# Kernel optimization log

Measured on AMD Instinct MI355X. Metric: run time of the kernel, lower is better.

The kernel has to match this reference:

```python
import jax, jax.numpy as jnp
import numpy as np

H = 128   # hidden_size
E = 100   # embedding/input_size
V = 1000  # vocabulary_size
FD = 512  # feature_extractor_dim
N, TQ, TA = 512, 64, 64


def _cell(x, h, c, Wih, Whh, b):
    # PyTorch LSTM cell, gate order i,f,g,o; b = b_ih + b_hh fused.
    z = x @ Wih.T + h @ Whh.T + b
    i, f, g, o = jnp.split(z, 4, axis=-1)
    c = jax.nn.sigmoid(f) * c + jax.nn.sigmoid(i) * jnp.tanh(g)
    h = jax.nn.sigmoid(o) * jnp.tanh(c)
    return h, c


def setup_inputs() -> dict:
    key = jax.random.key(0)
    ks = iter(jax.random.split(key, 40))
    def w(shape, s=0.08):
        return (s * jax.random.normal(next(ks), shape)).astype(jnp.float32)
    inp = {
        "questions": jax.random.randint(next(ks), (N, TQ), 0, V),
        "answers": jax.random.randint(next(ks), (N, TA), 0, V),
        "answer_lens": jax.random.randint(next(ks), (N,), 1, TA + 1),
        "img": w((FD,), 1.0),  # pre-extracted image features (feature_extractor = identity)
        "emb": w((V, E), 0.1),
    }
    for p in ("enc", "dec"):
        inp[p + "_Wih0"] = w((4 * H, E)); inp[p + "_Whh0"] = w((4 * H, H)); inp[p + "_b0"] = w((4 * H,))
        inp[p + "_Wih1"] = w((4 * H, H)); inp[p + "_Whh1"] = w((4 * H, H)); inp[p + "_b1"] = w((4 * H,))
    inp["Wk"] = w((H, H)); inp["bk"] = w((H,))
    inp["Wout"] = w((V, 3 * H + FD)); inp["bout"] = w((V,))
    return inp


def reference(questions, answers, answer_lens, img, emb,
              enc_Wih0, enc_Whh0, enc_b0, enc_Wih1, enc_Whh1, enc_b1,
              dec_Wih0, dec_Whh0, dec_b0, dec_Wih1, dec_Whh1, dec_b1,
              Wk, bk, Wout, bout):
    n, tq = questions.shape
    # ---- encode: 2-layer LSTM over all questions (batched), keys projection ----
    qe = emb[questions]                               # [N,TQ,E]
    z = jnp.zeros((n, H), emb.dtype)
    def enc_step(carry, x_t):
        h0, c0, h1, c1 = carry
        h0, c0 = _cell(x_t, h0, c0, enc_Wih0, enc_Whh0, enc_b0)
        h1, c1 = _cell(h0, h1, c1, enc_Wih1, enc_Whh1, enc_b1)
        return (h0, c0, h1, c1), h1
    (eh0, ec0, eh1, ec1), outs = jax.lax.scan(enc_step, (z, z, z, z), qe.swapaxes(0, 1))
    keys = outs.swapaxes(0, 1) @ Wk.T + bk            # [N,TQ,H]; decode uses keys as values too

    # ---- decode: sequential over questions (history carry), scan over timesteps ----
    ae = emb[answers]                                  # [N,TA,E]
    mask = (jnp.arange(answers.shape[1])[None, :] < answer_lens[:, None]).astype(emb.dtype)

    def q_step(history, xs):
        emb_q, k_q, h0, c0, h1, c1, m_q = xs
        def t_step(carry, x_t):
            h0, c0, h1, c1 = carry
            h0, c0 = _cell(x_t, h0, c0, dec_Wih0, dec_Whh0, dec_b0)
            h1, c1 = _cell(h0, h1, c1, dec_Wih1, dec_Whh1, dec_b1)
            ctx = jax.nn.softmax(k_q @ h1) @ k_q       # dot-product attention, v := k (as in source)
            feat = jnp.concatenate([h1, ctx, history, img], axis=-1)  # [3H+FD]
            return (h0, c0, h1, c1), feat @ Wout.T + bout
        carry, logits = jax.lax.scan(t_step, (h0, c0, h1, c1), emb_q)
        return carry[2], logits * m_q[:, None]         # history <- last-layer h; mask ragged tail

    _, logits = jax.lax.scan(q_step, jnp.zeros((H,), emb.dtype),
                             (ae, keys, eh0, ec0, eh1, ec1, mask))
    return logits                                      # [N,TA,V], zero-padded past answer_lens
```

## Files before the change

kernel.cpp:

```cpp
#include <hip/hip_runtime.h>
#include <stdint.h>

#define HD   128
#define ED   100
#define VD   1000
#define FDV  512
#define NS   512
#define TT   64
#define MT   (NS*TT)

typedef __attribute__((ext_vector_type(8))) short  short8;
typedef __attribute__((ext_vector_type(4))) float  f32x4;

typedef const __attribute__((address_space(1))) uint16_t* gas_u16;
typedef __attribute__((address_space(3))) uint16_t*       las_u16;

__device__ __forceinline__ float blo(uint32_t u){ return __uint_as_float(u << 16); }
__device__ __forceinline__ float bhi(uint32_t u){ return __uint_as_float(u & 0xffff0000u); }
__device__ __forceinline__ uint16_t f2bf(float f){
  uint32_t x = __float_as_uint(f);
  return (uint16_t)((x + 0x7fffu + ((x >> 16) & 1u)) >> 16);
}
__device__ __forceinline__ float sigf(float x){ return 1.f/(1.f+__expf(-x)); }
__device__ __forceinline__ float ftanh(float x){
  float ax = fabsf(x);
  float e = __expf(-2.f*ax);
  float t = (1.f - e) / (1.f + e);
  return copysignf(t, x);
}
__device__ __forceinline__ void lds_barrier(){
  asm volatile("s_waitcnt lgkmcnt(0)" ::: "memory");
  __builtin_amdgcn_s_barrier();
}

struct ConvJob { const float* s; uint16_t* d; int R, R0, C, Cp; };
struct ConvJobs { ConvJob j[12]; };

__global__ void k_convert(ConvJobs jobs){
  int stride = gridDim.x * blockDim.x;
  int tid0 = blockIdx.x * blockDim.x + threadIdx.x;
  for (int ji = 0; ji < 12; ++ji){
    const ConvJob jb = jobs.j[ji];
    int total = jb.R * jb.Cp;
    for (int i = tid0; i < total; i += stride){
      int r = i / jb.Cp, c = i - r*jb.Cp;
      float v = (r < jb.R0 && c < jb.C) ? jb.s[(size_t)r*jb.C + c] : 0.f;
      jb.d[i] = f2bf(v);
    }
  }
}

template<int MODE>
__global__ __launch_bounds__(256) void k_gemm(
    const uint16_t* __restrict__ A, const uint16_t* __restrict__ W,
    const float* __restrict__ bias, void* __restrict__ out,
    int N, int K, const int* __restrict__ lens, const int* __restrict__ tok)
{
  __shared__ __align__(16) uint16_t lsA[128][32];
  __shared__ __align__(16) uint16_t lsB[128][32];
  const int tid = threadIdx.x;
  const int n0 = blockIdx.x * 128, m0 = blockIdx.y * 128;
  const int l = tid & 63, w = tid >> 6;
  const int wm = (w >> 1) * 64, wn = (w & 1) * 64;
  const int fr = l & 15, fo = (l >> 4) * 8;
  const int srow = w*16 + (l >> 2);
  const int sce  = (l & 3) * 8;
  const int ar0 = m0 + srow, ar1 = m0 + 64 + srow;
  const size_t ab0 = (tok ? (size_t)tok[ar0] : (size_t)ar0) * K;
  const size_t ab1 = (tok ? (size_t)tok[ar1] : (size_t)ar1) * K;
  f32x4 acc[4][4] = {};
  for (int kt = 0; kt < K; kt += 32) {
    {
      __builtin_amdgcn_global_load_lds(
          (gas_u16)(A + ab0 + kt + sce),
          (las_u16)(&lsA[0][0] + w*512), 16, 0, 0);
      __builtin_amdgcn_global_load_lds(
          (gas_u16)(W + (size_t)(n0 + srow) * K + kt + sce),
          (las_u16)(&lsB[0][0] + w*512), 16, 0, 0);
      __builtin_amdgcn_global_load_lds(
          (gas_u16)(A + ab1 + kt + sce),
          (las_u16)(&lsA[0][0] + w*512 + 2048), 16, 0, 0);
      __builtin_amdgcn_global_load_lds(
          (gas_u16)(W + (size_t)(n0 + 64 + srow) * K + kt + sce),
          (las_u16)(&lsB[0][0] + w*512 + 2048), 16, 0, 0);
    }
    __syncthreads();
    short8 af[4], bfv[4];
    #pragma unroll
    for (int i = 0; i < 4; ++i) af[i]  = *(const short8*)(&lsA[wm + i*16 + fr][fo]);
    #pragma unroll
    for (int j = 0; j < 4; ++j) bfv[j] = *(const short8*)(&lsB[wn + j*16 + fr][fo]);
    #pragma unroll
    for (int i = 0; i < 4; ++i)
      #pragma unroll
      for (int j = 0; j < 4; ++j)
        acc[i][j] = __builtin_amdgcn_mfma_f32_16x16x32_bf16(af[i], bfv[j], acc[i][j], 0, 0, 0);
    __syncthreads();
  }
  const int r0 = (l >> 4) * 4, cc = l & 15;
  #pragma unroll
  for (int j = 0; j < 4; ++j) {
    int col = n0 + wn + j*16 + cc;
    if (col >= N) continue;
    float bv = bias[col];
    #pragma unroll
    for (int i = 0; i < 4; ++i) {
      #pragma unroll
      for (int r = 0; r < 4; ++r) {
        int row = m0 + wm + i*16 + r0 + r;
        float v = acc[i][j][r] + bv;
        if (MODE == 3) {
          int t = row & 63, n = row >> 6;
          size_t prow = ((size_t)(n >> 4)*64 + (size_t)t)*16 + (n & 15);
          ((uint16_t*)out)[prow * 512 + col] = f2bf(v);
        } else if (MODE == 2) {
          int t = row & 63, n = row >> 6;
          if (t >= lens[n]) v = 0.f;
          ((float*)out)[(size_t)row * N + col] = v;
        } else {
          ((float*)out)[(size_t)row * N + col] = v;
        }
      }
    }
  }
}

__global__ __launch_bounds__(512) void k_lstm_mfma(
    const uint16_t* __restrict__ X,
    const uint16_t* __restrict__ Whh,
    const float* __restrict__ h0i, const float* __restrict__ c0i,
    uint16_t* __restrict__ hout,
    float* __restrict__ hfin, float* __restrict__ cfin)
{
  __shared__ __align__(16) uint16_t hbuf[2][16][136];
  const int n0 = blockIdx.x * 16;
  const int w = threadIdx.x >> 6, l = threadIdx.x & 63;
  const int s = l & 15;
  const int hi4 = l >> 4;
  const int j0 = w*16 + hi4*4;

  short8 afr[4][4];
  #pragma unroll
  for (int g = 0; g < 4; ++g)
    #pragma unroll
    for (int kk = 0; kk < 4; ++kk)
      afr[g][kk] = *(const short8*)(Whh + (size_t)(g*128 + w*16 + s)*128 + kk*32 + hi4*8);

  f32x4 cst = {0.f, 0.f, 0.f, 0.f};
  if (c0i) cst = *(const f32x4*)(c0i + (size_t)(n0+s)*128 + j0);
  {
    uint16_t hb[4] = {0,0,0,0};
    if (h0i) {
      float4 hv = *(const float4*)(h0i + (size_t)(n0+s)*128 + j0);
      hb[0]=f2bf(hv.x); hb[1]=f2bf(hv.y); hb[2]=f2bf(hv.z); hb[3]=f2bf(hv.w);
    }
    *(uint2*)(&hbuf[0][s][j0]) = *(const uint2*)hb;
  }
  __syncthreads();

  const uint16_t* Xp = X + (size_t)blockIdx.x * TT * 8192 + s*512 + j0;
  uint2 xv[4], xvn[4];
  #pragma unroll
  for (int g = 0; g < 4; ++g) xv[g] = *(const uint2*)(Xp + g*128);

  float hfv[4] = {0.f,0.f,0.f,0.f};
  for (int t = 0; t < TT; ++t) {
    const int rb = t & 1;
    if (t + 1 < TT) {
      const uint16_t* Xn = Xp + (size_t)(t+1)*8192;
      #pragma unroll
      for (int g = 0; g < 4; ++g) xvn[g] = *(const uint2*)(Xn + g*128);
    }
    short8 bfr[4];
    #pragma unroll
    for (int kk = 0; kk < 4; ++kk)
      bfr[kk] = *(const short8*)(&hbuf[rb][s][kk*32 + hi4*8]);
    f32x4 acc[4] = {{0.f,0.f,0.f,0.f},{0.f,0.f,0.f,0.f},{0.f,0.f,0.f,0.f},{0.f,0.f,0.f,0.f}};
    #pragma unroll
    for (int kk = 0; kk < 4; ++kk)
      #pragma unroll
      for (int g = 0; g < 4; ++g)
        acc[g] = __builtin_amdgcn_mfma_f32_16x16x32_bf16(afr[g][kk], bfr[kk], acc[g], 0, 0, 0);
    uint16_t hb[4];
    #pragma unroll
    for (int r = 0; r < 4; ++r) {
      uint32_t wi = (r & 2) ? xv[0].y : xv[0].x;
      uint32_t wf = (r & 2) ? xv[1].y : xv[1].x;
      uint32_t wg = (r & 2) ? xv[2].y : xv[2].x;
      uint32_t wo = (r & 2) ? xv[3].y : xv[3].x;
      float zi = acc[0][r] + ((r & 1) ? bhi(wi) : blo(wi));
      float zf = acc[1][r] + ((r & 1) ? bhi(wf) : blo(wf));
      float zg = acc[2][r] + ((r & 1) ? bhi(wg) : blo(wg));
      float zo = acc[3][r] + ((r & 1) ? bhi(wo) : blo(wo));
      float cn = sigf(zf) * cst[r] + sigf(zi) * ftanh(zg);
      float h  = sigf(zo) * ftanh(cn);
      cst[r] = cn;
      hfv[r] = h;
      hb[r] = f2bf(h);
    }
    *(uint2*)(&hbuf[rb ^ 1][s][j0]) = *(const uint2*)hb;
    *(uint2*)(hout + ((size_t)(n0+s)*TT + t)*HD + j0) = *(const uint2*)hb;
    if (t + 1 < TT) {
      #pragma unroll
      for (int g = 0; g < 4; ++g) xv[g] = xvn[g];
    }
    lds_barrier();
  }
  if (hfin) *(float4*)(hfin + (size_t)(n0+s)*128 + j0) = make_float4(hfv[0],hfv[1],hfv[2],hfv[3]);
  if (cfin) *(float4*)(cfin + (size_t)(n0+s)*128 + j0) = make_float4(cst[0],cst[1],cst[2],cst[3]);
}

__global__ __launch_bounds__(256) void k_attn(
    const float* __restrict__ keys,
    const uint16_t* __restrict__ h1,
    const uint16_t* __restrict__ imgb,
    uint16_t* __restrict__ feat)
{
  __shared__ float ks[64][129];
  __shared__ float ps[4][64];
  const int n = blockIdx.x;
  for (int i = threadIdx.x; i < 64*128; i += 256)
    ks[i >> 7][i & 127] = keys[(size_t)n*8192 + i];
  const int w = threadIdx.x >> 6, l = threadIdx.x & 63;
  uint32_t hd = 0;
  if (n > 0) hd = ((const uint32_t*)(h1 + ((size_t)(n-1)*64 + 63)*128))[l];
  const uint4 iv = ((const uint4*)imgb)[l];
  __syncthreads();
  for (int tt = 0; tt < 16; ++tt) {
    const int t = tt*4 + w;
    const size_t m = (size_t)n*64 + t;
    const uint4* hp = (const uint4*)(h1 + m*128);
    float s = 0.f;
    #pragma unroll
    for (int k = 0; k < 16; ++k) {
      uint4 hv = hp[k];
      s += ks[l][8*k+0]*blo(hv.x) + ks[l][8*k+1]*bhi(hv.x)
         + ks[l][8*k+2]*blo(hv.y) + ks[l][8*k+3]*bhi(hv.y)
         + ks[l][8*k+4]*blo(hv.z) + ks[l][8*k+5]*bhi(hv.z)
         + ks[l][8*k+6]*blo(hv.w) + ks[l][8*k+7]*bhi(hv.w);
    }
    float mx = s;
    #pragma unroll
    for (int o = 32; o; o >>= 1) mx = fmaxf(mx, __shfl_xor(mx, o));
    float p = __expf(s - mx);
    float sm = p;
    #pragma unroll
    for (int o = 32; o; o >>= 1) sm += __shfl_xor(sm, o);
    p /= sm;
    ps[w][l] = p;
    float c0 = 0.f, c1 = 0.f;
    #pragma unroll
    for (int q = 0; q < 64; ++q) {
      float pq = ps[w][q];
      c0 += pq * ks[q][l];
      c1 += pq * ks[q][l + 64];
    }
    uint16_t* fr_ = feat + m*896;
    ((uint32_t*)fr_)[l] = ((const uint32_t*)(h1 + m*128))[l];
    fr_[128 + l] = f2bf(c0);
    fr_[192 + l] = f2bf(c1);
    ((uint32_t*)(fr_ + 256))[l] = hd;
    ((uint4*)(fr_ + 384))[l] = iv;
  }
}

extern "C" void kernel_launch(void* const* d_in, const int* in_sizes, int n_in,
                              void* d_out, int out_size, void* d_ws, size_t ws_size,
                              hipStream_t stream) {
  const int*   questions = (const int*)d_in[0];
  const int*   answers   = (const int*)d_in[1];
  const int*   lens      = (const int*)d_in[2];
  const float* img       = (const float*)d_in[3];
  const float* emb       = (const float*)d_in[4];
  const float* eWih0 = (const float*)d_in[5],  *eWhh0 = (const float*)d_in[6],  *eB0 = (const float*)d_in[7];
  const float* eWih1 = (const float*)d_in[8],  *eWhh1 = (const float*)d_in[9],  *eB1 = (const float*)d_in[10];
  const float* dWih0 = (const float*)d_in[11], *dWhh0 = (const float*)d_in[12], *dB0 = (const float*)d_in[13];
  const float* dWih1 = (const float*)d_in[14], *dWhh1 = (const float*)d_in[15], *dB1 = (const float*)d_in[16];
  const float* Wk   = (const float*)d_in[17], *bk   = (const float*)d_in[18];
  const float* Wout = (const float*)d_in[19], *bout = (const float*)d_in[20];

  char* ws = (char*)d_ws;
  size_t off = 0;
  auto alloc = [&](size_t n)->char* {
    char* p = ws + off; off += (n + 255) & ~(size_t)255; return p;
  };
  uint16_t* embP  = (uint16_t*)alloc((size_t)VD*128*2);
  uint16_t* wih0e = (uint16_t*)alloc(512*128*2);
  uint16_t* whh0e = (uint16_t*)alloc(512*128*2);
  uint16_t* wih1e = (uint16_t*)alloc(512*128*2);
  uint16_t* whh1e = (uint16_t*)alloc(512*128*2);
  uint16_t* wih0d = (uint16_t*)alloc(512*128*2);
  uint16_t* whh0d = (uint16_t*)alloc(512*128*2);
  uint16_t* wih1d = (uint16_t*)alloc(512*128*2);
  uint16_t* whh1d = (uint16_t*)alloc(512*128*2);
  uint16_t* wkb   = (uint16_t*)alloc(128*128*2);
  uint16_t* woutb = (uint16_t*)alloc((size_t)1024*896*2);
  uint16_t* imgb  = (uint16_t*)alloc(512*2);
  uint16_t* Xbuf  = (uint16_t*)alloc((size_t)MT*512*2);
  uint16_t* hA    = (uint16_t*)alloc((size_t)MT*128*2);
  uint16_t* h1b   = (uint16_t*)alloc((size_t)MT*128*2);
  float*    keysf = (float*)   alloc((size_t)MT*128*4);
  uint16_t* feat  = (uint16_t*)alloc((size_t)MT*896*2);
  float* eh0 = (float*)alloc(NS*128*4);
  float* ec0 = (float*)alloc(NS*128*4);
  float* eh1 = (float*)alloc(NS*128*4);
  float* ec1 = (float*)alloc(NS*128*4);
  if (off > ws_size) return;

  ConvJobs jobs;
  jobs.j[0]  = {emb,   embP,  VD,  VD,  ED,  128};
  jobs.j[1]  = {eWih0, wih0e, 512, 512, ED,  128};
  jobs.j[2]  = {eWhh0, whh0e, 512, 512, 128, 128};
  jobs.j[3]  = {eWih1, wih1e, 512, 512, 128, 128};
  jobs.j[4]  = {eWhh1, whh1e, 512, 512, 128, 128};
  jobs.j[5]  = {dWih0, wih0d, 512, 512, ED,  128};
  jobs.j[6]  = {dWhh0, whh0d, 512, 512, 128, 128};
  jobs.j[7]  = {dWih1, wih1d, 512, 512, 128, 128};
  jobs.j[8]  = {dWhh1, whh1d, 512, 512, 128, 128};
  jobs.j[9]  = {Wk,    wkb,   128, 128, 128, 128};
  jobs.j[10] = {Wout,  woutb, 1024, VD, 896, 896};
  jobs.j[11] = {img,   imgb,  1,   1,   512, 512};
  hipLaunchKernelGGL(k_convert, dim3(1024), dim3(256), 0, stream, jobs);

  hipLaunchKernelGGL(k_gemm<3>, dim3(4, MT/128), dim3(256), 0, stream, embP, wih0e, eB0, Xbuf, 512, 128, nullptr, questions);
  hipLaunchKernelGGL(k_lstm_mfma, dim3(NS/16), dim3(512), 0, stream, Xbuf, whh0e, (const float*)nullptr, (const float*)nullptr, hA, eh0, ec0);
  hipLaunchKernelGGL(k_gemm<3>, dim3(4, MT/128), dim3(256), 0, stream, hA, wih1e, eB1, Xbuf, 512, 128, nullptr, nullptr);
  hipLaunchKernelGGL(k_lstm_mfma, dim3(NS/16), dim3(512), 0, stream, Xbuf, whh1e, (const float*)nullptr, (const float*)nullptr, h1b, eh1, ec1);
  hipLaunchKernelGGL(k_gemm<0>, dim3(1, MT/128), dim3(256), 0, stream, h1b, wkb, bk, keysf, 128, 128, nullptr, nullptr);

  hipLaunchKernelGGL(k_gemm<3>, dim3(4, MT/128), dim3(256), 0, stream, embP, wih0d, dB0, Xbuf, 512, 128, nullptr, answers);
  hipLaunchKernelGGL(k_lstm_mfma, dim3(NS/16), dim3(512), 0, stream, Xbuf, whh0d, eh0, ec0, hA, (float*)nullptr, (float*)nullptr);
  hipLaunchKernelGGL(k_gemm<3>, dim3(4, MT/128), dim3(256), 0, stream, hA, wih1d, dB1, Xbuf, 512, 128, nullptr, nullptr);
  hipLaunchKernelGGL(k_lstm_mfma, dim3(NS/16), dim3(512), 0, stream, Xbuf, whh1d, eh1, ec1, h1b, (float*)nullptr, (float*)nullptr);

  hipLaunchKernelGGL(k_attn, dim3(NS), dim3(256), 0, stream, keysf, h1b, imgb, feat);
  hipLaunchKernelGGL(k_gemm<2>, dim3(8, MT/128), dim3(256), 0, stream, feat, woutb, bout, d_out, VD, 896, lens, nullptr);
}
```

Measured before the change: 890.7 us.

## Fuse both LSTM layers into one wavefront-pipelined recurrent kernel

Replaces the separate layer-0 LSTM, layer-1 input GEMM and layer-1 LSTM launches with a single kernel that runs both layers, skewed by one timestep. Each step computes layer 1 at t-1 from the layer-0 h already in LDS, so the layer-1 input projection is done in-kernel with register-resident Wih1 fragments. This removes the intermediate hA round-trip through global memory, one GEMM launch and one LSTM launch per encoder and decoder. In exchange it triples the weight fragments held in registers (occupancy/spill risk) and roughly doubles the MFMA work on each serial step. Final h states are now rounded through bf16.

```diff
diff --git a/kernel.cpp b/kernel.cpp
--- a/kernel.cpp
+++ b/kernel.cpp
@@ -125,89 +125,152 @@
   }
 }
 
-__global__ __launch_bounds__(512) void k_lstm_mfma(
+__global__ __launch_bounds__(512) void k_lstm2(
     const uint16_t* __restrict__ X,
-    const uint16_t* __restrict__ Whh,
+    const uint16_t* __restrict__ Whh0,
+    const uint16_t* __restrict__ Wih1,
+    const uint16_t* __restrict__ Whh1,
+    const float* __restrict__ B1,
     const float* __restrict__ h0i, const float* __restrict__ c0i,
+    const float* __restrict__ h1i, const float* __restrict__ c1i,
     uint16_t* __restrict__ hout,
-    float* __restrict__ hfin, float* __restrict__ cfin)
+    float* __restrict__ h0f, float* __restrict__ c0f,
+    float* __restrict__ h1f, float* __restrict__ c1f)
 {
-  __shared__ __align__(16) uint16_t hbuf[2][16][136];
+  __shared__ __align__(16) uint16_t hb0[2][16][136];
+  __shared__ __align__(16) uint16_t hb1[2][16][136];
   const int n0 = blockIdx.x * 16;
   const int w = threadIdx.x >> 6, l = threadIdx.x & 63;
   const int s = l & 15;
   const int hi4 = l >> 4;
   const int j0 = w*16 + hi4*4;
 
-  short8 afr[4][4];
+  short8 w0fr[4][4], wi1fr[4][4], wh1fr[4][4];
   #pragma unroll
   for (int g = 0; g < 4; ++g)
     #pragma unroll
-    for (int kk = 0; kk < 4; ++kk)
-      afr[g][kk] = *(const short8*)(Whh + (size_t)(g*128 + w*16 + s)*128 + kk*32 + hi4*8);
-
-  f32x4 cst = {0.f, 0.f, 0.f, 0.f};
-  if (c0i) cst = *(const f32x4*)(c0i + (size_t)(n0+s)*128 + j0);
+    for (int kk = 0; kk < 4; ++kk) {
+      const size_t ro = (size_t)(g*128 + w*16 + s)*128 + kk*32 + hi4*8;
+      w0fr[g][kk]  = *(const short8*)(Whh0 + ro);
+      wi1fr[g][kk] = *(const short8*)(Wih1 + ro);
+      wh1fr[g][kk] = *(const short8*)(Whh1 + ro);
+    }
+  f32x4 b1v[4];
+  #pragma unroll
+  for (int g = 0; g < 4; ++g) b1v[g] = *(const f32x4*)(B1 + g*128 + j0);
+
+  f32x4 cst0 = {0.f,0.f,0.f,0.f}, cst1 = {0.f,0.f,0.f,0.f};
+  if (c0i) cst0 = *(const f32x4*)(c0i + (size_t)(n0+s)*128 + j0);
+  if (c1i) cst1 = *(const f32x4*)(c1i + (size_t)(n0+s)*128 + j0);
   {
-    uint16_t hb[4] = {0,0,0,0};
+    uint16_t a[4] = {0,0,0,0}, b[4] = {0,0,0,0};
     if (h0i) {
       float4 hv = *(const float4*)(h0i + (size_t)(n0+s)*128 + j0);
-      hb[0]=f2bf(hv.x); hb[1]=f2bf(hv.y); hb[2]=f2bf(hv.z); hb[3]=f2bf(hv.w);
-    }
-    *(uint2*)(&hbuf[0][s][j0]) = *(const uint2*)hb;
+      a[0]=f2bf(hv.x); a[1]=f2bf(hv.y); a[2]=f2bf(hv.z); a[3]=f2bf(hv.w);
+    }
+    if (h1i) {
+      float4 hv = *(const float4*)(h1i + (size_t)(n0+s)*128 + j0);
+      b[0]=f2bf(hv.x); b[1]=f2bf(hv.y); b[2]=f2bf(hv.z); b[3]=f2bf(hv.w);
+    }
+    *(uint2*)(&hb0[1][s][j0]) = *(const uint2*)a;
+    *(uint2*)(&hb1[1][s][j0]) = *(const uint2*)b;
   }
   __syncthreads();
 
   const uint16_t* Xp = X + (size_t)blockIdx.x * TT * 8192 + s*512 + j0;
-  uint2 xv[4], xvn[4];
+  uint16_t* hop = hout + (size_t)(n0+s)*TT*HD + j0;
+
+  uint2 xv[4];
   #pragma unroll
   for (int g = 0; g < 4; ++g) xv[g] = *(const uint2*)(Xp + g*128);
 
-  float hfv[4] = {0.f,0.f,0.f,0.f};
-  for (int t = 0; t < TT; ++t) {
-    const int rb = t & 1;
-    if (t + 1 < TT) {
-      const uint16_t* Xn = Xp + (size_t)(t+1)*8192;
-      #pragma unroll
-      for (int g = 0; g < 4; ++g) xvn[g] = *(const uint2*)(Xn + g*128);
-    }
-    short8 bfr[4];
+  for (int t = 0; t <= TT; ++t) {
+    const int ra = (t+1)&1, wa = t&1;
+    short8 bfr0[4];
     #pragma unroll
     for (int kk = 0; kk < 4; ++kk)
-      bfr[kk] = *(const short8*)(&hbuf[rb][s][kk*32 + hi4*8]);
-    f32x4 acc[4] = {{0.f,0.f,0.f,0.f},{0.f,0.f,0.f,0.f},{0.f,0.f,0.f,0.f},{0.f,0.f,0.f,0.f}};
-    #pragma unroll
-    for (int kk = 0; kk < 4; ++kk)
-      #pragma unroll
-      for (int g = 0; g < 4; ++g)
-        acc[g] = __builtin_amdgcn_mfma_f32_16x16x32_bf16(afr[g][kk], bfr[kk], acc[g], 0, 0, 0);
-    uint16_t hb[4];
-    #pragma unroll
-    for (int r = 0; r < 4; ++r) {
-      uint32_t wi = (r & 2) ? xv[0].y : xv[0].x;
-      uint32_t wf = (r & 2) ? xv[1].y : xv[1].x;
-      uint32_t wg = (r & 2) ? xv[2].y : xv[2].x;
-      uint32_t wo = (r & 2) ? xv[3].y : xv[3].x;
-      float zi = acc[0][r] + ((r & 1) ? bhi(wi) : blo(wi));
-      float zf = acc[1][r] + ((r & 1) ? bhi(wf) : blo(wf));
-      float zg = acc[2][r] + ((r & 1) ? bhi(wg) : blo(wg));
-      float zo = acc[3][r] + ((r & 1) ? bhi(wo) : blo(wo));
-      float cn = sigf(zf) * cst[r] + sigf(zi) * ftanh(zg);
-      float h  = sigf(zo) * ftanh(cn);
-      cst[r] = cn;
-      hfv[r] = h;
-      hb[r] = f2bf(h);
-    }
-    *(uint2*)(&hbuf[rb ^ 1][s][j0]) = *(const uint2*)hb;
-    *(uint2*)(hout + ((size_t)(n0+s)*TT + t)*HD + j0) = *(const uint2*)hb;
-    if (t + 1 < TT) {
-      #pragma unroll
-      for (int g = 0; g < 4; ++g) xv[g] = xvn[g];
+      bfr0[kk] = *(const short8*)(&hb0[ra][s][kk*32 + hi4*8]);
+
+    f32x4 acc1[4] = {{0,0,0,0},{0,0,0,0},{0,0,0,0},{0,0,0,0}};
+    if (t > 0) {
+      short8 bfr1[4];
+      #pragma unroll
+      for (int kk = 0; kk < 4; ++kk)
+        bfr1[kk] = *(const short8*)(&hb1[wa][s][kk*32 + hi4*8]);
+      #pragma unroll
+      for (int kk = 0; kk < 4; ++kk)
+        #pragma unroll
+        for (int g = 0; g < 4; ++g)
+          acc1[g] = __builtin_amdgcn_mfma_f32_16x16x32_bf16(wh1fr[g][kk], bfr1[kk], acc1[g], 0, 0, 0);
+      #pragma unroll
+      for (int kk = 0; kk < 4; ++kk)
+        #pragma unroll
+        for (int g = 0; g < 4; ++g)
+          acc1[g] = __builtin_amdgcn_mfma_f32_16x16x32_bf16(wi1fr[g][kk], bfr0[kk], acc1[g], 0, 0, 0);
+    }
+    f32x4 acc0[4] = {{0,0,0,0},{0,0,0,0},{0,0,0,0},{0,0,0,0}};
+    if (t < TT) {
+      #pragma unroll
+      for (int kk = 0; kk < 4; ++kk)
+        #pragma unroll
+        for (int g = 0; g < 4; ++g)
+          acc0[g] = __builtin_amdgcn_mfma_f32_16x16x32_bf16(w0fr[g][kk], bfr0[kk], acc0[g], 0, 0, 0);
+    }
+    if (t > 0) {
+      uint16_t hb[4];
+      #pragma unroll
+      for (int r = 0; r < 4; ++r) {
+        float zi = acc1[0][r] + b1v[0][r];
+        float zf = acc1[1][r] + b1v[1][r];
+        float zg = acc1[2][r] + b1v[2][r];
+        float zo = acc1[3][r] + b1v[3][r];
+        float cn = sigf(zf) * cst1[r] + sigf(zi) * ftanh(zg);
+        float h  = sigf(zo) * ftanh(cn);
+        cst1[r] = cn;
+        hb[r] = f2bf(h);
+      }
+      *(uint2*)(&hb1[ra][s][j0]) = *(const uint2*)hb;
+      *(uint2*)(hop + (size_t)(t-1)*HD) = *(const uint2*)hb;
+    }
+    if (t < TT) {
+      uint16_t hb[4];
+      #pragma unroll
+      for (int r = 0; r < 4; ++r) {
+        uint32_t wi = (r & 2) ? xv[0].y : xv[0].x;
+        uint32_t wf = (r & 2) ? xv[1].y : xv[1].x;
+        uint32_t wg = (r & 2) ? xv[2].y : xv[2].x;
+        uint32_t wo = (r & 2) ? xv[3].y : xv[3].x;
+        float zi = acc0[0][r] + ((r & 1) ? bhi(wi) : blo(wi));
+        float zf = acc0[1][r] + ((r & 1) ? bhi(wf) : blo(wf));
+        float zg = acc0[2][r] + ((r & 1) ? bhi(wg) : blo(wg));
+        float zo = acc0[3][r] + ((r & 1) ? bhi(wo) : blo(wo));
+        float cn = sigf(zf) * cst0[r] + sigf(zi) * ftanh(zg);
+        float h  = sigf(zo) * ftanh(cn);
+        cst0[r] = cn;
+        hb[r] = f2bf(h);
+      }
+      *(uint2*)(&hb0[wa][s][j0]) = *(const uint2*)hb;
+      if (t + 1 < TT) {
+        const uint16_t* Xn = Xp + (size_t)(t+1)*8192;
+        #pragma unroll
+        for (int g = 0; g < 4; ++g) xv[g] = *(const uint2*)(Xn + g*128);
+      }
     }
     lds_barrier();
   }
-  if (hfin) *(float4*)(hfin + (size_t)(n0+s)*128 + j0) = make_float4(hfv[0],hfv[1],hfv[2],hfv[3]);
-  if (cfin) *(float4*)(cfin + (size_t)(n0+s)*128 + j0) = make_float4(cst[0],cst[1],cst[2],cst[3]);
+
+  if (h0f) {
+    uint2 a = *(const uint2*)(&hb0[1][s][j0]);
+    uint2 b = *(const uint2*)(&hb1[1][s][j0]);
+    const uint16_t* ap = (const uint16_t*)&a;
+    const uint16_t* bp = (const uint16_t*)&b;
+    float4 h0v = make_float4(blo(ap[0]), blo(ap[1]), blo(ap[2]), blo(ap[3]));
+    float4 h1v = make_float4(blo(bp[0]), blo(bp[1]), blo(bp[2]), blo(bp[3]));
+    *(float4*)(h0f + (size_t)(n0+s)*128 + j0) = h0v;
+    *(float4*)(h1f + (size_t)(n0+s)*128 + j0) = h1v;
+    *(f32x4*)(c0f + (size_t)(n0+s)*128 + j0) = cst0;
+    *(f32x4*)(c1f + (size_t)(n0+s)*128 + j0) = cst1;
+  }
 }
 
 __global__ __launch_bounds__(256) void k_attn(
@@ -297,7 +360,6 @@
   uint16_t* woutb = (uint16_t*)alloc((size_t)1024*896*2);
   uint16_t* imgb  = (uint16_t*)alloc(512*2);
   uint16_t* Xbuf  = (uint16_t*)alloc((size_t)MT*512*2);
-  uint16_t* hA    = (uint16_t*)alloc((size_t)MT*128*2);
   uint16_t* h1b   = (uint16_t*)alloc((size_t)MT*128*2);
   float*    keysf = (float*)   alloc((size_t)MT*128*4);
   uint16_t* feat  = (uint16_t*)alloc((size_t)MT*896*2);
@@ -323,15 +385,17 @@
   hipLaunchKernelGGL(k_convert, dim3(1024), dim3(256), 0, stream, jobs);
 
   hipLaunchKernelGGL(k_gemm<3>, dim3(4, MT/128), dim3(256), 0, stream, embP, wih0e, eB0, Xbuf, 512, 128, nullptr, questions);
-  hipLaunchKernelGGL(k_lstm_mfma, dim3(NS/16), dim3(512), 0, stream, Xbuf, whh0e, (const float*)nullptr, (const float*)nullptr, hA, eh0, ec0);
-  hipLaunchKernelGGL(k_gemm<3>, dim3(4, MT/128), dim3(256), 0, stream, hA, wih1e, eB1, Xbuf, 512, 128, nullptr, nullptr);
-  hipLaunchKernelGGL(k_lstm_mfma, dim3(NS/16), dim3(512), 0, stream, Xbuf, whh1e, (const float*)nullptr, (const float*)nullptr, h1b, eh1, ec1);
+  hipLaunchKernelGGL(k_lstm2, dim3(NS/16), dim3(512), 0, stream,
+                     Xbuf, whh0e, wih1e, whh1e, eB1,
+                     (const float*)nullptr, (const float*)nullptr, (const float*)nullptr, (const float*)nullptr,
+                     h1b, eh0, ec0, eh1, ec1);
   hipLaunchKernelGGL(k_gemm<0>, dim3(1, MT/128), dim3(256), 0, stream, h1b, wkb, bk, keysf, 128, 128, nullptr, nullptr);
 
   hipLaunchKernelGGL(k_gemm<3>, dim3(4, MT/128), dim3(256), 0, stream, embP, wih0d, dB0, Xbuf, 512, 128, nullptr, answers);
-  hipLaunchKernelGGL(k_lstm_mfma, dim3(NS/16), dim3(512), 0, stream, Xbuf, whh0d, eh0, ec0, hA, (float*)nullptr, (float*)nullptr);
-  hipLaunchKernelGGL(k_gemm<3>, dim3(4, MT/128), dim3(256), 0, stream, hA, wih1d, dB1, Xbuf, 512, 128, nullptr, nullptr);
-  hipLaunchKernelGGL(k_lstm_mfma, dim3(NS/16), dim3(512), 0, stream, Xbuf, whh1d, eh1, ec1, h1b, (float*)nullptr, (float*)nullptr);
+  hipLaunchKernelGGL(k_lstm2, dim3(NS/16), dim3(512), 0, stream,
+                     Xbuf, whh0d, wih1d, whh1d, dB1,
+                     eh0, ec0, eh1, ec1,
+                     h1b, (float*)nullptr, (float*)nullptr, (float*)nullptr, (float*)nullptr);
 
   hipLaunchKernelGGL(k_attn, dim3(NS), dim3(256), 0, stream, keysf, h1b, imgb, feat);
   hipLaunchKernelGGL(k_gemm<2>, dim3(8, MT/128), dim3(256), 0, stream, feat, woutb, bout, d_out, VD, 896, lens, nullptr);
```

After: 1.033 ms. 16.0% more time.

## Process two interleaved sequence groups per LSTM block to hide recurrence latency

Applied to the files above, without the earlier changes.

The recurrent LSTM kernel now has each block handle 32 sequences as two independent 16-row groups. Their MFMA chains and gate math are interleaved so each group's dependent latency can hide the other's, and the time loop is unrolled by two with a double-buffered X prefetch. This halves the grid to 16 blocks, leaving fewer CUs busy, and raises register pressure. Whether per-step latency hiding beats the lost parallelism is uncertain.

```diff
diff --git a/kernel.cpp b/kernel.cpp
--- a/kernel.cpp
+++ b/kernel.cpp
@@ -125,18 +125,96 @@
   }
 }
 
-__global__ __launch_bounds__(512) void k_lstm_mfma(
+template<int RB>
+__device__ __forceinline__ void lstm_step(
+    const short8 (&afr)[4][4],
+    uint16_t (*hb)[2][16][136],
+    int s, int hi4, int j0, int t,
+    const uint16_t* __restrict__ XA, const uint16_t* __restrict__ XB,
+    uint2 (&xa)[4], uint2 (&xb)[4],
+    f32x4& cstA, f32x4& cstB,
+    uint16_t* __restrict__ hoA, uint16_t* __restrict__ hoB,
+    float (&hfA)[4], float (&hfB)[4])
+{
+  short8 bA[4], bB[4];
+  #pragma unroll
+  for (int kk = 0; kk < 4; ++kk) {
+    bA[kk] = *(const short8*)(&hb[RB][0][s][kk*32 + hi4*8]);
+    bB[kk] = *(const short8*)(&hb[RB][1][s][kk*32 + hi4*8]);
+  }
+  f32x4 aA[4] = {{0,0,0,0},{0,0,0,0},{0,0,0,0},{0,0,0,0}};
+  f32x4 aB[4] = {{0,0,0,0},{0,0,0,0},{0,0,0,0},{0,0,0,0}};
+  #pragma unroll
+  for (int kk = 0; kk < 4; ++kk) {
+    #pragma unroll
+    for (int g = 0; g < 4; ++g)
+      aA[g] = __builtin_amdgcn_mfma_f32_16x16x32_bf16(afr[g][kk], bA[kk], aA[g], 0, 0, 0);
+    #pragma unroll
+    for (int g = 0; g < 4; ++g)
+      aB[g] = __builtin_amdgcn_mfma_f32_16x16x32_bf16(afr[g][kk], bB[kk], aB[g], 0, 0, 0);
+  }
+  {
+    uint16_t hv[4];
+    #pragma unroll
+    for (int r = 0; r < 4; ++r) {
+      uint32_t wi = (r & 2) ? xa[0].y : xa[0].x;
+      uint32_t wf = (r & 2) ? xa[1].y : xa[1].x;
+      uint32_t wg = (r & 2) ? xa[2].y : xa[2].x;
+      uint32_t wo = (r & 2) ? xa[3].y : xa[3].x;
+      float zi = aA[0][r] + ((r & 1) ? bhi(wi) : blo(wi));
+      float zf = aA[1][r] + ((r & 1) ? bhi(wf) : blo(wf));
+      float zg = aA[2][r] + ((r & 1) ? bhi(wg) : blo(wg));
+      float zo = aA[3][r] + ((r & 1) ? bhi(wo) : blo(wo));
+      float cn = sigf(zf) * cstA[r] + sigf(zi) * ftanh(zg);
+      float h  = sigf(zo) * ftanh(cn);
+      cstA[r] = cn; hfA[r] = h; hv[r] = f2bf(h);
+    }
+    *(uint2*)(&hb[RB ^ 1][0][s][j0]) = *(const uint2*)hv;
+    *(uint2*)(hoA + (size_t)t*HD) = *(const uint2*)hv;
+    if (t + 2 < TT) {
+      const uint16_t* Xn = XA + (size_t)(t+2)*8192;
+      #pragma unroll
+      for (int g = 0; g < 4; ++g) xa[g] = *(const uint2*)(Xn + g*128);
+    }
+  }
+  {
+    uint16_t hv[4];
+    #pragma unroll
+    for (int r = 0; r < 4; ++r) {
+      uint32_t wi = (r & 2) ? xb[0].y : xb[0].x;
+      uint32_t wf = (r & 2) ? xb[1].y : xb[1].x;
+      uint32_t wg = (r & 2) ? xb[2].y : xb[2].x;
+      uint32_t wo = (r & 2) ? xb[3].y : xb[3].x;
+      float zi = aB[0][r] + ((r & 1) ? bhi(wi) : blo(wi));
+      float zf = aB[1][r] + ((r & 1) ? bhi(wf) : blo(wf));
+      float zg = aB[2][r] + ((r & 1) ? bhi(wg) : blo(wg));
+      float zo = aB[3][r] + ((r & 1) ? bhi(wo) : blo(wo));
+      float cn = sigf(zf) * cstB[r] + sigf(zi) * ftanh(zg);
+      float h  = sigf(zo) * ftanh(cn);
+      cstB[r] = cn; hfB[r] = h; hv[r] = f2bf(h);
+    }
+    *(uint2*)(&hb[RB ^ 1][1][s][j0]) = *(const uint2*)hv;
+    *(uint2*)(hoB + (size_t)t*HD) = *(const uint2*)hv;
+    if (t + 2 < TT) {
+      const uint16_t* Xn = XB + (size_t)(t+2)*8192;
+      #pragma unroll
+      for (int g = 0; g < 4; ++g) xb[g] = *(const uint2*)(Xn + g*128);
+    }
+  }
+  lds_barrier();
+}
+
+__global__ __launch_bounds__(512, 2) void k_lstm_d(
     const uint16_t* __restrict__ X,
     const uint16_t* __restrict__ Whh,
     const float* __restrict__ h0i, const float* __restrict__ c0i,
     uint16_t* __restrict__ hout,
     float* __restrict__ hfin, float* __restrict__ cfin)
 {
-  __shared__ __align__(16) uint16_t hbuf[2][16][136];
-  const int n0 = blockIdx.x * 16;
+  __shared__ __align__(16) uint16_t hbuf[2][2][16][136];
+  const int b = blockIdx.x;
   const int w = threadIdx.x >> 6, l = threadIdx.x & 63;
-  const int s = l & 15;
-  const int hi4 = l >> 4;
+  const int s = l & 15, hi4 = l >> 4;
   const int j0 = w*16 + hi4*4;
 
   short8 afr[4][4];
@@ -146,68 +224,49 @@
     for (int kk = 0; kk < 4; ++kk)
       afr[g][kk] = *(const short8*)(Whh + (size_t)(g*128 + w*16 + s)*128 + kk*32 + hi4*8);
 
-  f32x4 cst = {0.f, 0.f, 0.f, 0.f};
-  if (c0i) cst = *(const f32x4*)(c0i + (size_t)(n0+s)*128 + j0);
+  const int nA = b*32 + s, nB = b*32 + 16 + s;
+  f32x4 cstA = {0,0,0,0}, cstB = {0,0,0,0};
+  if (c0i) {
+    cstA = *(const f32x4*)(c0i + (size_t)nA*128 + j0);
+    cstB = *(const f32x4*)(c0i + (size_t)nB*128 + j0);
+  }
   {
-    uint16_t hb[4] = {0,0,0,0};
+    uint16_t ha[4] = {0,0,0,0}, hc[4] = {0,0,0,0};
     if (h0i) {
-      float4 hv = *(const float4*)(h0i + (size_t)(n0+s)*128 + j0);
-      hb[0]=f2bf(hv.x); hb[1]=f2bf(hv.y); hb[2]=f2bf(hv.z); hb[3]=f2bf(hv.w);
-    }
-    *(uint2*)(&hbuf[0][s][j0]) = *(const uint2*)hb;
+      float4 v = *(const float4*)(h0i + (size_t)nA*128 + j0);
+      ha[0]=f2bf(v.x); ha[1]=f2bf(v.y); ha[2]=f2bf(v.z); ha[3]=f2bf(v.w);
+      float4 u = *(const float4*)(h0i + (size_t)nB*128 + j0);
+      hc[0]=f2bf(u.x); hc[1]=f2bf(u.y); hc[2]=f2bf(u.z); hc[3]=f2bf(u.w);
+    }
+    *(uint2*)(&hbuf[0][0][s][j0]) = *(const uint2*)ha;
+    *(uint2*)(&hbuf[0][1][s][j0]) = *(const uint2*)hc;
   }
   __syncthreads();
 
-  const uint16_t* Xp = X + (size_t)blockIdx.x * TT * 8192 + s*512 + j0;
-  uint2 xv[4], xvn[4];
+  const uint16_t* XA = X + (size_t)(2*b)*TT*8192 + (size_t)s*512 + j0;
+  const uint16_t* XB = XA + (size_t)TT*8192;
+  uint2 xA0[4], xA1[4], xB0[4], xB1[4];
   #pragma unroll
-  for (int g = 0; g < 4; ++g) xv[g] = *(const uint2*)(Xp + g*128);
-
-  float hfv[4] = {0.f,0.f,0.f,0.f};
-  for (int t = 0; t < TT; ++t) {
-    const int rb = t & 1;
-    if (t + 1 < TT) {
-      const uint16_t* Xn = Xp + (size_t)(t+1)*8192;
-      #pragma unroll
-      for (int g = 0; g < 4; ++g) xvn[g] = *(const uint2*)(Xn + g*128);
-    }
-    short8 bfr[4];
-    #pragma unroll
-    for (int kk = 0; kk < 4; ++kk)
-      bfr[kk] = *(const short8*)(&hbuf[rb][s][kk*32 + hi4*8]);
-    f32x4 acc[4] = {{0.f,0.f,0.f,0.f},{0.f,0.f,0.f,0.f},{0.f,0.f,0.f,0.f},{0.f,0.f,0.f,0.f}};
-    #pragma unroll
-    for (int kk = 0; kk < 4; ++kk)
-      #pragma unroll
-      for (int g = 0; g < 4; ++g)
-        acc[g] = __builtin_amdgcn_mfma_f32_16x16x32_bf16(afr[g][kk], bfr[kk], acc[g], 0, 0, 0);
-    uint16_t hb[4];
-    #pragma unroll
-    for (int r = 0; r < 4; ++r) {
-      uint32_t wi = (r & 2) ? xv[0].y : xv[0].x;
-      uint32_t wf = (r & 2) ? xv[1].y : xv[1].x;
-      uint32_t wg = (r & 2) ? xv[2].y : xv[2].x;
-      uint32_t wo = (r & 2) ? xv[3].y : xv[3].x;
-      float zi = acc[0][r] + ((r & 1) ? bhi(wi) : blo(wi));
-      float zf = acc[1][r] + ((r & 1) ? bhi(wf) : blo(wf));
-      float zg = acc[2][r] + ((r & 1) ? bhi(wg) : blo(wg));
-      float zo = acc[3][r] + ((r & 1) ? bhi(wo) : blo(wo));
-      float cn = sigf(zf) * cst[r] + sigf(zi) * ftanh(zg);
-      float h  = sigf(zo) * ftanh(cn);
-      cst[r] = cn;
-      hfv[r] = h;
-      hb[r] = f2bf(h);
-    }
-    *(uint2*)(&hbuf[rb ^ 1][s][j0]) = *(const uint2*)hb;
-    *(uint2*)(hout + ((size_t)(n0+s)*TT + t)*HD + j0) = *(const uint2*)hb;
-    if (t + 1 < TT) {
-      #pragma unroll
-      for (int g = 0; g < 4; ++g) xv[g] = xvn[g];
-    }
-    lds_barrier();
-  }
-  if (hfin) *(float4*)(hfin + (size_t)(n0+s)*128 + j0) = make_float4(hfv[0],hfv[1],hfv[2],hfv[3]);
-  if (cfin) *(float4*)(cfin + (size_t)(n0+s)*128 + j0) = make_float4(cst[0],cst[1],cst[2],cst[3]);
+  for (int g = 0; g < 4; ++g) {
+    xA0[g] = *(const uint2*)(XA + g*128);
+    xA1[g] = *(const uint2*)(XA + 8192 + g*128);
+    xB0[g] = *(const uint2*)(XB + g*128);
+    xB1[g] = *(const uint2*)(XB + 8192 + g*128);
+  }
+  uint16_t* hoA = hout + (size_t)nA*TT*HD + j0;
+  uint16_t* hoB = hout + (size_t)nB*TT*HD + j0;
+
+  float hfA[4] = {0,0,0,0}, hfB[4] = {0,0,0,0};
+  for (int t = 0; t < TT; t += 2) {
+    lstm_step<0>(afr, hbuf, s, hi4, j0, t,   XA, XB, xA0, xB0, cstA, cstB, hoA, hoB, hfA, hfB);
+    lstm_step<1>(afr, hbuf, s, hi4, j0, t+1, XA, XB, xA1, xB1, cstA, cstB, hoA, hoB, hfA, hfB);
+  }
+  if (hfin) {
+    *(float4*)(hfin + (size_t)nA*128 + j0) = make_float4(hfA[0],hfA[1],hfA[2],hfA[3]);
+    *(float4*)(hfin + (size_t)nB*128 + j0) = make_float4(hfB[0],hfB[1],hfB[2],hfB[3]);
+    *(f32x4*)(cfin + (size_t)nA*128 + j0) = cstA;
+    *(f32x4*)(cfin + (size_t)nB*128 + j0) = cstB;
+  }
 }
 
 __global__ __launch_bounds__(256) void k_attn(
@@ -323,15 +382,19 @@
   hipLaunchKernelGGL(k_convert, dim3(1024), dim3(256), 0, stream, jobs);
 
   hipLaunchKernelGGL(k_gemm<3>, dim3(4, MT/128), dim3(256), 0, stream, embP, wih0e, eB0, Xbuf, 512, 128, nullptr, questions);
-  hipLaunchKernelGGL(k_lstm_mfma, dim3(NS/16), dim3(512), 0, stream, Xbuf, whh0e, (const float*)nullptr, (const float*)nullptr, hA, eh0, ec0);
+  hipLaunchKernelGGL(k_lstm_d, dim3(NS/32), dim3(512), 0, stream, Xbuf, whh0e,
+                     (const float*)nullptr, (const float*)nullptr, hA, eh0, ec0);
   hipLaunchKernelGGL(k_gemm<3>, dim3(4, MT/128), dim3(256), 0, stream, hA, wih1e, eB1, Xbuf, 512, 128, nullptr, nullptr);
-  hipLaunchKernelGGL(k_lstm_mfma, dim3(NS/16), dim3(512), 0, stream, Xbuf, whh1e, (const float*)nullptr, (const float*)nullptr, h1b, eh1, ec1);
+  hipLaunchKernelGGL(k_lstm_d, dim3(NS/32), dim3(512), 0, stream, Xbuf, whh1e,
+                     (const float*)nullptr, (const float*)nullptr, h1b, eh1, ec1);
   hipLaunchKernelGGL(k_gemm<0>, dim3(1, MT/128), dim3(256), 0, stream, h1b, wkb, bk, keysf, 128, 128, nullptr, nullptr);
 
   hipLaunchKernelGGL(k_gemm<3>, dim3(4, MT/128), dim3(256), 0, stream, embP, wih0d, dB0, Xbuf, 512, 128, nullptr, answers);
-  hipLaunchKernelGGL(k_lstm_mfma, dim3(NS/16), dim3(512), 0, stream, Xbuf, whh0d, eh0, ec0, hA, (float*)nullptr, (float*)nullptr);
+  hipLaunchKernelGGL(k_lstm_d, dim3(NS/32), dim3(512), 0, stream, Xbuf, whh0d,
+                     eh0, ec0, hA, (float*)nullptr, (float*)nullptr);
   hipLaunchKernelGGL(k_gemm<3>, dim3(4, MT/128), dim3(256), 0, stream, hA, wih1d, dB1, Xbuf, 512, 128, nullptr, nullptr);
-  hipLaunchKernelGGL(k_lstm_mfma, dim3(NS/16), dim3(512), 0, stream, Xbuf, whh1d, eh1, ec1, h1b, (float*)nullptr, (float*)nullptr);
+  hipLaunchKernelGGL(k_lstm_d, dim3(NS/32), dim3(512), 0, stream, Xbuf, whh1d,
+                     eh1, ec1, h1b, (float*)nullptr, (float*)nullptr);
 
   hipLaunchKernelGGL(k_attn, dim3(NS), dim3(256), 0, stream, keysf, h1b, imgb, feat);
   hipLaunchKernelGGL(k_gemm<2>, dim3(8, MT/128), dim3(256), 0, stream, feat, woutb, bout, d_out, VD, 896, lens, nullptr);
```

Result: slower. 1.404 ms (+57.7%).
